# Optimization experiments

Measured on AMD Instinct MI355X. Metric: run time of the kernel, lower is better.

Reference implementation:

```python
import jax, jax.numpy as jnp
import numpy as np

NUM_CLASSES = 90
NUM_ANCHORS = 9          # 3 octaves x 3 aspect ratios
MAX_DETECTION_POINTS = 5000
MAX_DET_PER_IMAGE = 100
SIGMA = 0.5              # gaussian soft-NMS sigma
IMAGE_SIZE = 512
LEVEL_HW = [64, 32, 16, 8, 4]   # levels 3..7, stride 8..128
BATCH = 16


def _make_anchors():
    """effdet-style anchors, [N,4] in (y1,x1,y2,x2) pixel coords, per-location
    anchor-contiguous ordering (matches permute(0,2,3,1) flattening)."""
    boxes_all = []
    for level in range(3, 8):
        stride = 2 ** level
        boxes_level = []
        for octave in range(3):
            for aspect in (1.0, 2.0, 0.5):
                base = 4.0 * stride * 2.0 ** (octave / 3.0)  # anchor_scale=4
                ax = np.sqrt(aspect)
                ay = 1.0 / ax
                hx = base * ax / 2.0
                hy = base * ay / 2.0
                xs = np.arange(stride / 2.0, IMAGE_SIZE, stride)
                xv, yv = np.meshgrid(xs, xs)
                b = np.stack([yv - hy, xv - hx, yv + hy, xv + hx], axis=-1)
                boxes_level.append(b.reshape(-1, 1, 4))
        boxes_all.append(np.concatenate(boxes_level, axis=1).reshape(-1, 4))
    return np.concatenate(boxes_all, axis=0).astype(np.float32)


def setup_inputs() -> dict:
    key = jax.random.key(0)
    ks = jax.random.split(key, 10)
    inp = {}
    for i, hw in enumerate(LEVEL_HW):
        inp[f"cls_l{i}"] = jax.random.normal(ks[i], (BATCH, NUM_ANCHORS * NUM_CLASSES, hw, hw), jnp.float32)
        inp[f"box_l{i}"] = jax.random.normal(ks[5 + i], (BATCH, NUM_ANCHORS * 4, hw, hw), jnp.float32) * 0.1
    inp["anchors"] = jnp.asarray(_make_anchors())
    return inp


def _flatten_level(t, c):
    # [B, A*c, H, W] -> [B, H*W*A, c]
    B, _, H, W = t.shape
    return jnp.transpose(t, (0, 2, 3, 1)).reshape(B, H * W * NUM_ANCHORS, c)


def _iou(box, boxes):
    # box [4], boxes [N,4], xyxy
    x1 = jnp.maximum(box[0], boxes[:, 0])
    y1 = jnp.maximum(box[1], boxes[:, 1])
    x2 = jnp.minimum(box[2], boxes[:, 2])
    y2 = jnp.minimum(box[3], boxes[:, 3])
    inter = jnp.clip(x2 - x1, 0.0) * jnp.clip(y2 - y1, 0.0)
    a1 = (box[2] - box[0]) * (box[3] - box[1])
    a2 = (boxes[:, 2] - boxes[:, 0]) * (boxes[:, 3] - boxes[:, 1])
    return inter / (a1 + a2 - inter + 1e-8)


def _soft_nms(bx, sc, cl):
    # gaussian soft-NMS: iteratively pick max score, decay neighbours.
    def step(sc_work, _):
        i = jnp.argmax(sc_work)
        s = sc_work[i]
        ious = _iou(bx[i], bx)
        decay = jnp.exp(-(ious * ious) / SIGMA)
        sc_new = (sc_work * decay).at[i].set(-jnp.inf)
        return sc_new, (i, s)

    _, (idxs, sels) = jax.lax.scan(step, sc, None, length=MAX_DET_PER_IMAGE)
    # detections [max_det, 6] = x1,y1,x2,y2,score,class
    return jnp.concatenate(
        [bx[idxs], sels[:, None], cl[idxs].astype(jnp.float32)[:, None]], axis=1)


def reference(cls_l0, cls_l1, cls_l2, cls_l3, cls_l4,
              box_l0, box_l1, box_l2, box_l3, box_l4, anchors):
    cls_levels = [cls_l0, cls_l1, cls_l2, cls_l3, cls_l4]
    box_levels = [box_l0, box_l1, box_l2, box_l3, box_l4]
    B = cls_l0.shape[0]

    cls_all = jnp.concatenate([_flatten_level(t, NUM_CLASSES) for t in cls_levels], 1)  # [B,N,C]
    box_all = jnp.concatenate([_flatten_level(t, 4) for t in box_levels], 1)            # [B,N,4]

    # top-k over flattened anchor*class logits (effdet _post_process)
    top_scores, top_idx = jax.lax.top_k(cls_all.reshape(B, -1), MAX_DETECTION_POINTS)
    anchor_idx = top_idx // NUM_CLASSES    # [B,K]
    classes = top_idx % NUM_CLASSES        # [B,K]

    rel = jnp.take_along_axis(box_all, anchor_idx[..., None], axis=1)  # [B,K,4]
    anc = anchors[anchor_idx]                                          # [B,K,4] (y1,x1,y2,x2)
    scores = jax.nn.sigmoid(top_scores)

    # decode (effdet decode_box_outputs, output xyxy)
    ya = (anc[..., 0] + anc[..., 2]) * 0.5
    xa = (anc[..., 1] + anc[..., 3]) * 0.5
    ha = anc[..., 2] - anc[..., 0]
    wa = anc[..., 3] - anc[..., 1]
    ty, tx, th, tw = rel[..., 0], rel[..., 1], rel[..., 2], rel[..., 3]
    w = jnp.exp(tw) * wa
    h = jnp.exp(th) * ha
    yc = ty * ha + ya
    xc = tx * wa + xa
    boxes = jnp.stack([xc - w * 0.5, yc - h * 0.5, xc + w * 0.5, yc + h * 0.5], -1)

    return jax.vmap(_soft_nms)(boxes, scores, classes)  # [B, max_det, 6]
```

## Files before the change

### kernel.cpp

```cpp
#include <hip/hip_runtime.h>
#include <math.h>

#define K_TOP   5000
#define M_HOT   2048
#define NHOT    2560
#define NSEL2   5632
#define MAX_DET 100
#define CAP     16384
#define SCAP    384
#define NSH     64
#define TAU     2.8f
#define BATCH   16

__device__ __forceinline__ unsigned f2u(float x) {
    unsigned b = __float_as_uint(x);
    return (b & 0x80000000u) ? ~b : (b | 0x80000000u);
}
__device__ __forceinline__ float u2f(unsigned u) {
    unsigned b = (u & 0x80000000u) ? (u & 0x7fffffffu) : ~u;
    return __uint_as_float(b);
}

__global__ __launch_bounds__(256) void k_compact(
    const float* __restrict__ c0, const float* __restrict__ c1,
    const float* __restrict__ c2, const float* __restrict__ c3,
    const float* __restrict__ c4,
    unsigned* __restrict__ ctr, uint2* __restrict__ cbuf)
{
    const unsigned V0 = 13271040u, V1 = 16588800u, V2 = 17418240u,
                   V3 = 17625600u, V4 = 17677440u;
    unsigned tid  = threadIdx.x;
    unsigned lane = tid & 63u;
    unsigned wid  = tid >> 6;
    unsigned shard = (blockIdx.x * 4u + wid) & (NSH - 1u);
    unsigned gbase = blockIdx.x * 2048u + tid;

    #pragma unroll 1
    for (int it = 0; it < 8; it++) {
        unsigned g = gbase + (unsigned)it * 256u;
        bool valid = (g < V4);
        const float* p; unsigned vbase, lgHW, lgW, aoff;
        if (g < V0)      { p = c0; vbase = 0;  lgHW = 12; lgW = 6; aoff = 0; }
        else if (g < V1) { p = c1; vbase = V0; lgHW = 10; lgW = 5; aoff = 36864u; }
        else if (g < V2) { p = c2; vbase = V1; lgHW = 8;  lgW = 4; aoff = 46080u; }
        else if (g < V3) { p = c3; vbase = V2; lgHW = 6;  lgW = 3; aoff = 48384u; }
        else             { p = c4; vbase = V3; lgHW = 4;  lgW = 2; aoff = 48960u; }

        unsigned us[4], fl[4];
        int m = 0;
        unsigned b = 0;
        if (valid) {
            unsigned elem = (g - vbase) << 2;
            unsigned pos  = elem & ((1u << lgHW) - 1u);
            unsigned q    = elem >> lgHW;
            b             = q / 810u;
            unsigned ch   = q - b * 810u;
            unsigned a    = ch / 90u;
            unsigned c    = ch - a * 90u;
            unsigned h    = pos >> lgW;
            unsigned w0   = pos & ((1u << lgW) - 1u);
            float4 v = *(const float4*)(p + elem);
            unsigned anch = aoff + ((h << lgW) + w0) * 9u + a;
            float vv[4] = {v.x, v.y, v.z, v.w};
            #pragma unroll
            for (int k = 0; k < 4; k++) {
                if (vv[k] > TAU) {
                    us[m] = f2u(vv[k]);
                    fl[m] = (anch + (unsigned)k * 9u) * 90u + c;
                    m++;
                }
            }
        }

        unsigned bb  = valid ? b : 0xffffffffu;
        unsigned b0u = (unsigned)__shfl((int)bb, 0);
        unsigned long long same = __ballot(bb == b0u);
        if (same == ~0ULL) {
            unsigned long long B[4];
            int cnt[4];
            #pragma unroll
            for (int k = 0; k < 4; k++) { B[k] = __ballot(m > k); cnt[k] = __popcll(B[k]); }
            int tot = cnt[0] + cnt[1] + cnt[2] + cnt[3];
            if (tot > 0) {
                unsigned base = 0;
                if (lane == 0)
                    base = atomicAdd(&ctr[(b0u * NSH + shard) * 16u], (unsigned)tot);
                base = (unsigned)__shfl((int)base, 0);
                unsigned long long below = (lane == 0) ? 0ULL : ((1ULL << lane) - 1ULL);
                unsigned lb = 0;
                #pragma unroll
                for (int k = 0; k < 4; k++) {
                    if (k < m) {
                        unsigned o = base + lb + (unsigned)__popcll(B[k] & below);
                        if (o < SCAP)
                            cbuf[((size_t)b0u * NSH + shard) * SCAP + o] = make_uint2(us[k], fl[k]);
                    }
                    lb += (unsigned)cnt[k];
                }
            }
        } else {
            for (int k = 0; k < m; k++) {
                unsigned o = atomicAdd(&ctr[(b * NSH + shard) * 16u], 1u);
                if (o < SCAP)
                    cbuf[((size_t)b * NSH + shard) * SCAP + o] = make_uint2(us[k], fl[k]);
            }
        }
    }
}

__global__ __launch_bounds__(1024) void k_select(
    const uint2* __restrict__ cbuf, const unsigned* __restrict__ ctr,
    uint2* __restrict__ tmp,
    const float* __restrict__ b0p, const float* __restrict__ b1p,
    const float* __restrict__ b2p, const float* __restrict__ b3p,
    const float* __restrict__ b4p, const float* __restrict__ anchors,
    float* __restrict__ sx1, float* __restrict__ sy1,
    float* __restrict__ sx2, float* __restrict__ sy2,
    float* __restrict__ ssc, float* __restrict__ scl,
    unsigned* __restrict__ su, unsigned* __restrict__ sfl,
    float* __restrict__ u2sig_arr)
{
    int img = blockIdx.x;
    int tid = threadIdx.x;
    unsigned lane = (unsigned)tid & 63u;
    __shared__ unsigned hist[256];
    __shared__ unsigned scnt[NSH], spref[NSH];
    __shared__ unsigned sTot;
    __shared__ unsigned sPrefix, sNeed;
    __shared__ unsigned cE, cH, cC;

    for (int i = tid; i < NSEL2; i += 1024) {
        size_t o = (size_t)img * NSEL2 + i;
        ssc[o] = -INFINITY;
        sx1[o] = 0.f; sy1[o] = 0.f; sx2[o] = 0.f; sy2[o] = 0.f; scl[o] = 0.f;
        su[o] = 0u; sfl[o] = 0xffffffffu;
    }

    if (tid < NSH) {
        unsigned c = ctr[((unsigned)img * NSH + (unsigned)tid) * 16u];
        scnt[tid] = (c > SCAP) ? SCAP : c;
    }
    __syncthreads();
    if (tid == 0) {
        unsigned s = 0;
        for (int i = 0; i < NSH; i++) { spref[i] = s; s += scnt[i]; }
        sTot = (s > CAP) ? CAP : s;
    }
    __syncthreads();
    for (unsigned idx = (unsigned)tid; idx < NSH * SCAP; idx += 1024u) {
        unsigned sh = idx / SCAP, j = idx - sh * SCAP;
        if (j < scnt[sh]) {
            unsigned dst = spref[sh] + j;
            if (dst < CAP)
                tmp[(size_t)img * CAP + dst] = cbuf[((size_t)img * NSH + sh) * SCAP + j];
        }
    }
    __syncthreads();
    unsigned n = sTot;
    const uint2* buf = tmp + (size_t)img * CAP;

    unsigned uthr[2], needArr[2];
    #pragma unroll 1
    for (int si = 0; si < 2; si++) {
        unsigned prefix = 0, need = (si == 0) ? K_TOP : M_HOT;
        for (int r = 0; r < 4; r++) {
            int sh = 24 - 8 * r;
            for (int i = tid; i < 256; i += 1024) hist[i] = 0;
            __syncthreads();
            for (unsigned i0 = 0; i0 < n; i0 += 1024) {
                unsigned i = i0 + (unsigned)tid;
                bool vld = false; unsigned bin = 0;
                if (i < n) {
                    unsigned u = buf[i].x;
                    vld = (r == 0) || ((u >> (sh + 8)) == prefix);
                    bin = (u >> sh) & 0xffu;
                }
                unsigned long long act = __ballot(vld);
                if (act) {
                    int fa = __ffsll(act) - 1;
                    unsigned fb = (unsigned)__shfl((int)bin, fa);
                    unsigned long long sm = __ballot(vld && (bin == fb));
                    if (sm == act) {
                        if ((int)lane == fa) atomicAdd(&hist[fb], (unsigned)__popcll(act));
                    } else if (vld) {
                        atomicAdd(&hist[bin], 1u);
                    }
                }
            }
            __syncthreads();
            if (tid == 0) {
                unsigned s = 0; int bin = 255;
                for (; bin > 0; bin--) {
                    unsigned t = s + hist[bin];
                    if (t >= need) break;
                    s = t;
                }
                sPrefix = (prefix << 8) | (unsigned)bin;
                sNeed   = need - s;
            }
            __syncthreads();
            prefix = sPrefix;
            need   = sNeed;
        }
        uthr[si] = prefix; needArr[si] = need;
    }
    unsigned u_star = uthr[0], needEq = needArr[0];
    unsigned u2key  = uthr[1];
    if (n <= K_TOP) { u_star = 0; needEq = K_TOP; }
    if (n <= M_HOT) { u2key = 0; }

    if (tid == 0) {
        cE = 0; cH = 0; cC = 0;
        u2sig_arr[img] = (n > M_HOT) ? 1.0f / (1.0f + expf(-u2f(u2key))) : -1.0f;
    }
    __syncthreads();

    for (unsigned i0 = 0; i0 < n; i0 += 1024) {
        unsigned i = i0 + (unsigned)tid;
        unsigned u = 0, fx = 0;
        bool gt = false, eq = false;
        if (i < n) {
            uint2 e = buf[i];
            u = e.x; fx = e.y;
            gt = (u > u_star);
            eq = (u == u_star);
        }
        bool win = gt;
        unsigned long long me = __ballot(eq);
        if (me) {
            int leader = __ffsll(me) - 1;
            unsigned base = 0;
            if ((int)lane == leader) base = atomicAdd(&cE, (unsigned)__popcll(me));
            base = (unsigned)__shfl((int)base, leader);
            if (eq) {
                unsigned qd = base + (unsigned)__popcll(me & ((1ULL << lane) - 1ULL));
                if (qd < needEq) win = true;
            }
        }
        bool hot = win && (u >= u2key);
        unsigned dest = 0xffffffffu;
        bool spill = false;
        unsigned long long mh = __ballot(hot);
        if (mh) {
            int leader = __ffsll(mh) - 1;
            unsigned base = 0;
            if ((int)lane == leader) base = atomicAdd(&cH, (unsigned)__popcll(mh));
            base = (unsigned)__shfl((int)base, leader);
            if (hot) {
                unsigned hq = base + (unsigned)__popcll(mh & ((1ULL << lane) - 1ULL));
                if (hq < NHOT) dest = hq; else spill = true;
            }
        }
        bool cold = win && (!hot || spill);
        unsigned long long mc = __ballot(cold);
        if (mc) {
            int leader = __ffsll(mc) - 1;
            unsigned base = 0;
            if ((int)lane == leader) base = atomicAdd(&cC, (unsigned)__popcll(mc));
            base = (unsigned)__shfl((int)base, leader);
            if (cold) dest = NHOT + base + (unsigned)__popcll(mc & ((1ULL << lane) - 1ULL));
        }
        if (win && dest < NSEL2) {
            unsigned anchor = fx / 90u;
            unsigned c      = fx - anchor * 90u;
            const float* bp; unsigned off, lgW;
            if (anchor < 36864u)      { bp = b0p; off = 0;      lgW = 6; }
            else if (anchor < 46080u) { bp = b1p; off = 36864u; lgW = 5; }
            else if (anchor < 48384u) { bp = b2p; off = 46080u; lgW = 4; }
            else if (anchor < 48960u) { bp = b3p; off = 48384u; lgW = 3; }
            else                      { bp = b4p; off = 48960u; lgW = 2; }
            unsigned il   = anchor - off;
            unsigned a    = il % 9u;
            unsigned ppos = il / 9u;
            unsigned w    = ppos & ((1u << lgW) - 1u);
            unsigned h    = ppos >> lgW;
            unsigned HW   = 1u << (2 * lgW);
            size_t base_i = ((size_t)((unsigned)img * 36u + a * 4u) << (2 * lgW))
                            + ((size_t)h << lgW) + w;
            float ty  = bp[base_i];
            float tx  = bp[base_i + HW];
            float th  = bp[base_i + 2 * (size_t)HW];
            float tw_ = bp[base_i + 3 * (size_t)HW];
            float4 anc = ((const float4*)anchors)[anchor];
            float ya = (anc.x + anc.z) * 0.5f;
            float xa = (anc.y + anc.w) * 0.5f;
            float ha = anc.z - anc.x;
            float wa = anc.w - anc.y;
            float wb = expf(tw_) * wa;
            float hb = expf(th)  * ha;
            float yc = ty * ha + ya;
            float xc = tx * wa + xa;
            float logit = u2f(u);
            float score = 1.0f / (1.0f + expf(-logit));
            size_t o = (size_t)img * NSEL2 + dest;
            sx1[o] = xc - wb * 0.5f;
            sy1[o] = yc - hb * 0.5f;
            sx2[o] = xc + wb * 0.5f;
            sy2[o] = yc + hb * 0.5f;
            ssc[o] = score;
            scl[o] = (float)c;
            su[o]  = u;
            sfl[o] = fx;
        }
    }
}

template<int NS>
__device__ __forceinline__ float nms_run(
    const float* __restrict__ sx1, const float* __restrict__ sy1,
    const float* __restrict__ sx2, const float* __restrict__ sy2,
    const float* __restrict__ ssc, const float* __restrict__ scl,
    const unsigned* __restrict__ su, const unsigned* __restrict__ sfl,
    float* __restrict__ out, int img,
    float* shv, int* shs, unsigned long long* shk, float* bbx)
{
    int tid = threadIdx.x;
    unsigned lane = (unsigned)tid & 63u;
    unsigned wid  = (unsigned)tid >> 6;

    float x1[NS], y1[NS], x2[NS], y2[NS], sc[NS], cl[NS], ar[NS];
    unsigned long long kk[NS];
    size_t base = (size_t)img * NSEL2;
    #pragma unroll
    for (int j = 0; j < NS; j++) {
        int s = tid + j * 256;
        x1[j] = sx1[base + s]; y1[j] = sy1[base + s];
        x2[j] = sx2[base + s]; y2[j] = sy2[base + s];
        sc[j] = ssc[base + s]; cl[j] = scl[base + s];
        kk[j] = ((unsigned long long)su[base + s] << 32)
              | (unsigned long long)(0xffffffffu - sfl[base + s]);
        ar[j] = (x2[j] - x1[j]) * (y2[j] - y1[j]);
    }

    float last = -INFINITY;
    for (int it = 0; it < MAX_DET; it++) {
        float v = sc[0]; int s = tid; unsigned long long k = kk[0];
        #pragma unroll
        for (int j = 1; j < NS; j++) {
            if (sc[j] > v || (sc[j] == v && kk[j] > k)) {
                v = sc[j]; s = tid + j * 256; k = kk[j];
            }
        }
        #pragma unroll
        for (int d = 32; d; d >>= 1) {
            float v2 = __shfl_down(v, d);
            int   s2 = __shfl_down(s, d);
            unsigned long long k2 = __shfl_down(k, d);
            if (v2 > v || (v2 == v && k2 > k)) { v = v2; s = s2; k = k2; }
        }
        if (lane == 0) { shv[wid] = v; shs[wid] = s; shk[wid] = k; }
        __syncthreads();
        v = shv[0]; s = shs[0]; k = shk[0];
        #pragma unroll
        for (int w = 1; w < 4; w++) {
            float v2 = shv[w]; int s2 = shs[w]; unsigned long long k2 = shk[w];
            if (v2 > v || (v2 == v && k2 > k)) { v = v2; s = s2; k = k2; }
        }
        int ot = s & 255, oj = s >> 8;
        if (tid == ot) {
            float* bx = bbx;
            #pragma unroll
            for (int j = 0; j < NS; j++) {
                if (j == oj) {
                    bx[0] = x1[j]; bx[1] = y1[j]; bx[2] = x2[j]; bx[3] = y2[j];
                    bx[4] = cl[j];
                    sc[j] = -INFINITY;
                }
            }
        }
        __syncthreads();
        float gx1 = bbx[0], gy1 = bbx[1], gx2 = bbx[2], gy2 = bbx[3];
        if (tid == 0) {
            float* o = out + ((size_t)img * MAX_DET + it) * 6;
            o[0] = gx1; o[1] = gy1; o[2] = gx2; o[3] = gy2;
            o[4] = v;  o[5] = bbx[4];
        }
        last = v;
        float ga = (gx2 - gx1) * (gy2 - gy1);
        #pragma unroll
        for (int j = 0; j < NS; j++) {
            float xx1 = fmaxf(gx1, x1[j]);
            float yy1 = fmaxf(gy1, y1[j]);
            float xx2 = fminf(gx2, x2[j]);
            float yy2 = fminf(gy2, y2[j]);
            float inter = fmaxf(xx2 - xx1, 0.f) * fmaxf(yy2 - yy1, 0.f);
            float iou = inter / (ga + ar[j] - inter + 1e-8f);
            sc[j] *= expf(-2.0f * iou * iou);
        }
    }
    return last;
}

__global__ __launch_bounds__(256) void k_nms(
    const float* __restrict__ sx1, const float* __restrict__ sy1,
    const float* __restrict__ sx2, const float* __restrict__ sy2,
    const float* __restrict__ ssc, const float* __restrict__ scl,
    const unsigned* __restrict__ su, const unsigned* __restrict__ sfl,
    const float* __restrict__ u2sig_arr,
    float* __restrict__ out)
{
    __shared__ float shv[4];
    __shared__ int shs[4];
    __shared__ unsigned long long shk[4];
    __shared__ float bbx[5];
    int img = blockIdx.x;

    float s100 = nms_run<10>(sx1, sy1, sx2, sy2, ssc, scl, su, sfl,
                             out, img, shv, shs, shk, bbx);
    float u2s = u2sig_arr[img];
    if (!(s100 > u2s)) {
        __syncthreads();
        nms_run<22>(sx1, sy1, sx2, sy2, ssc, scl, su, sfl,
                    out, img, shv, shs, shk, bbx);
    }
}

extern "C" void kernel_launch(void* const* d_in, const int* in_sizes, int n_in,
                              void* d_out, int out_size, void* d_ws, size_t ws_size,
                              hipStream_t stream)
{
    const float* cls[5] = {0,0,0,0,0};
    const float* box[5] = {0,0,0,0,0};
    const float* anchors = 0;
    const int cls_sz[5] = {53084160, 13271040, 3317760, 829440, 207360};
    const int box_sz[5] = {2359296, 589824, 147456, 36864, 9216};
    for (int i = 0; i < n_in; i++) {
        int sz = in_sizes[i];
        const float* p = (const float*)d_in[i];
        if (sz == 196416) { anchors = p; continue; }
        for (int l = 0; l < 5; l++) {
            if (sz == cls_sz[l]) { cls[l] = p; break; }
            if (sz == box_sz[l]) { box[l] = p; break; }
        }
    }
    float* out = (float*)d_out;

    char* ws = (char*)d_ws;
    unsigned* ctr = (unsigned*)ws;
    size_t off = (size_t)BATCH * NSH * 16 * sizeof(unsigned);
    float* u2sig = (float*)(ws + off);
    off += 256;
    uint2* cbuf = (uint2*)(ws + off);
    off += (size_t)BATCH * NSH * SCAP * sizeof(uint2);
    uint2* tmp = (uint2*)(ws + off);
    off += (size_t)BATCH * CAP * sizeof(uint2);
    float* sel = (float*)(ws + off);
    float* sx1 = sel;
    float* sy1 = sel + 1 * (size_t)BATCH * NSEL2;
    float* sx2 = sel + 2 * (size_t)BATCH * NSEL2;
    float* sy2 = sel + 3 * (size_t)BATCH * NSEL2;
    float* ssc = sel + 4 * (size_t)BATCH * NSEL2;
    float* scl = sel + 5 * (size_t)BATCH * NSEL2;
    unsigned* su  = (unsigned*)(sel + 6 * (size_t)BATCH * NSEL2);
    unsigned* sfl = (unsigned*)(sel + 7 * (size_t)BATCH * NSEL2);

    hipMemsetAsync(ctr, 0, (size_t)BATCH * NSH * 16 * sizeof(unsigned), stream);
    k_compact<<<dim3(8632), dim3(256), 0, stream>>>(cls[0], cls[1], cls[2], cls[3], cls[4],
                                                    ctr, cbuf);
    k_select<<<dim3(BATCH), dim3(1024), 0, stream>>>(cbuf, ctr, tmp,
                                                     box[0], box[1], box[2], box[3], box[4],
                                                     anchors,
                                                     sx1, sy1, sx2, sy2, ssc, scl, su, sfl,
                                                     u2sig);
    k_nms<<<dim3(BATCH), dim3(256), 0, stream>>>(sx1, sy1, sx2, sy2, ssc, scl, su, sfl,
                                                 u2sig, out);
}
```

Measured before the change: 730.7 us.

## Run hot-set soft-NMS in a single wavefront with DPP argmax reduction

The fast-path soft-NMS now runs in one 64-lane wavefront per image, holding a smaller hot candidate set (M_HOT 2048 to 1024) in registers. The argmax uses DPP cross-lane ops and readlane broadcasts, which removes the LDS round-trips and __syncthreads per iteration. The fallback full-set NMS moves to a separate kernel gated by a per-image flag, at the cost of an extra launch and higher register pressure (17 slots of 9 arrays per lane). A smaller hot set may also trigger the fallback more often, and the fallback is costly.

```diff
diff --git a/kernel.cpp b/kernel.cpp
--- a/kernel.cpp
+++ b/kernel.cpp
@@ -2,9 +2,11 @@
 #include <math.h>
 
 #define K_TOP   5000
-#define M_HOT   2048
-#define NHOT    2560
-#define NSEL2   5632
+#define M_HOT   1024
+#define NHOT    1088
+#define NSEL2   5696
+#define NS_HOT  17
+#define NS_FIX  23
 #define MAX_DET 100
 #define CAP     16384
 #define SCAP    384
@@ -305,80 +307,87 @@
     }
 }
 
-template<int NS>
-__device__ __forceinline__ float nms_run(
+template<int CTRL, int RM>
+__device__ __forceinline__ void dpp_amax(float& v, int& s, unsigned& kh, unsigned& kl) {
+    float v2 = __int_as_float(__builtin_amdgcn_update_dpp(
+        __float_as_int(v), __float_as_int(v), CTRL, RM, 0xf, false));
+    int s2 = __builtin_amdgcn_update_dpp(s, s, CTRL, RM, 0xf, false);
+    unsigned h2 = (unsigned)__builtin_amdgcn_update_dpp((int)kh, (int)kh, CTRL, RM, 0xf, false);
+    unsigned l2 = (unsigned)__builtin_amdgcn_update_dpp((int)kl, (int)kl, CTRL, RM, 0xf, false);
+    bool better = (v2 > v) || (v2 == v && (h2 > kh || (h2 == kh && l2 > kl)));
+    if (better) { v = v2; s = s2; kh = h2; kl = l2; }
+}
+
+__global__ __launch_bounds__(64) void k_nms(
     const float* __restrict__ sx1, const float* __restrict__ sy1,
     const float* __restrict__ sx2, const float* __restrict__ sy2,
     const float* __restrict__ ssc, const float* __restrict__ scl,
     const unsigned* __restrict__ su, const unsigned* __restrict__ sfl,
-    float* __restrict__ out, int img,
-    float* shv, int* shs, unsigned long long* shk, float* bbx)
+    const float* __restrict__ u2sig_arr, unsigned* __restrict__ flags,
+    float* __restrict__ out)
 {
+    int img = blockIdx.x;
     int tid = threadIdx.x;
-    unsigned lane = (unsigned)tid & 63u;
-    unsigned wid  = (unsigned)tid >> 6;
-
-    float x1[NS], y1[NS], x2[NS], y2[NS], sc[NS], cl[NS], ar[NS];
-    unsigned long long kk[NS];
+
+    float x1[NS_HOT], y1[NS_HOT], x2[NS_HOT], y2[NS_HOT], sc[NS_HOT], cl[NS_HOT], ar[NS_HOT];
+    unsigned kh[NS_HOT], kl[NS_HOT];
     size_t base = (size_t)img * NSEL2;
     #pragma unroll
-    for (int j = 0; j < NS; j++) {
-        int s = tid + j * 256;
+    for (int j = 0; j < NS_HOT; j++) {
+        int s = tid + j * 64;
         x1[j] = sx1[base + s]; y1[j] = sy1[base + s];
         x2[j] = sx2[base + s]; y2[j] = sy2[base + s];
         sc[j] = ssc[base + s]; cl[j] = scl[base + s];
-        kk[j] = ((unsigned long long)su[base + s] << 32)
-              | (unsigned long long)(0xffffffffu - sfl[base + s]);
+        kh[j] = su[base + s];  kl[j] = ~sfl[base + s];
         ar[j] = (x2[j] - x1[j]) * (y2[j] - y1[j]);
     }
 
     float last = -INFINITY;
+    #pragma unroll 1
     for (int it = 0; it < MAX_DET; it++) {
-        float v = sc[0]; int s = tid; unsigned long long k = kk[0];
-        #pragma unroll
-        for (int j = 1; j < NS; j++) {
-            if (sc[j] > v || (sc[j] == v && kk[j] > k)) {
-                v = sc[j]; s = tid + j * 256; k = kk[j];
-            }
-        }
-        #pragma unroll
-        for (int d = 32; d; d >>= 1) {
-            float v2 = __shfl_down(v, d);
-            int   s2 = __shfl_down(s, d);
-            unsigned long long k2 = __shfl_down(k, d);
-            if (v2 > v || (v2 == v && k2 > k)) { v = v2; s = s2; k = k2; }
-        }
-        if (lane == 0) { shv[wid] = v; shs[wid] = s; shk[wid] = k; }
-        __syncthreads();
-        v = shv[0]; s = shs[0]; k = shk[0];
-        #pragma unroll
-        for (int w = 1; w < 4; w++) {
-            float v2 = shv[w]; int s2 = shs[w]; unsigned long long k2 = shk[w];
-            if (v2 > v || (v2 == v && k2 > k)) { v = v2; s = s2; k = k2; }
-        }
-        int ot = s & 255, oj = s >> 8;
-        if (tid == ot) {
-            float* bx = bbx;
-            #pragma unroll
-            for (int j = 0; j < NS; j++) {
-                if (j == oj) {
-                    bx[0] = x1[j]; bx[1] = y1[j]; bx[2] = x2[j]; bx[3] = y2[j];
-                    bx[4] = cl[j];
-                    sc[j] = -INFINITY;
-                }
-            }
-        }
-        __syncthreads();
-        float gx1 = bbx[0], gy1 = bbx[1], gx2 = bbx[2], gy2 = bbx[3];
-        if (tid == 0) {
+        float v = sc[0]; int s = tid; unsigned bh = kh[0], bl = kl[0];
+        #pragma unroll
+        for (int j = 1; j < NS_HOT; j++) {
+            bool better = (sc[j] > v) ||
+                          (sc[j] == v && (kh[j] > bh || (kh[j] == bh && kl[j] > bl)));
+            if (better) { v = sc[j]; s = tid + j * 64; bh = kh[j]; bl = kl[j]; }
+        }
+        dpp_amax<0x111, 0xf>(v, s, bh, bl);
+        dpp_amax<0x112, 0xf>(v, s, bh, bl);
+        dpp_amax<0x114, 0xf>(v, s, bh, bl);
+        dpp_amax<0x118, 0xf>(v, s, bh, bl);
+        dpp_amax<0x142, 0xa>(v, s, bh, bl);
+        dpp_amax<0x143, 0xc>(v, s, bh, bl);
+
+        int wslot = __builtin_amdgcn_readlane(s, 63);
+        float wv  = __int_as_float(__builtin_amdgcn_readlane(__float_as_int(v), 63));
+        wslot = __builtin_amdgcn_readfirstlane(wslot);
+        int wj    = wslot >> 6;
+        int owner = wslot & 63;
+
+        float rx1 = 0.f, ry1 = 0.f, rx2 = 0.f, ry2 = 0.f, rcl = 0.f;
+        #pragma unroll
+        for (int j = 0; j < NS_HOT; j++) {
+            if (j == wj) {
+                rx1 = x1[j]; ry1 = y1[j]; rx2 = x2[j]; ry2 = y2[j]; rcl = cl[j];
+                if (tid == owner) sc[j] = -INFINITY;
+            }
+        }
+        float gx1 = __int_as_float(__builtin_amdgcn_readlane(__float_as_int(rx1), owner));
+        float gy1 = __int_as_float(__builtin_amdgcn_readlane(__float_as_int(ry1), owner));
+        float gx2 = __int_as_float(__builtin_amdgcn_readlane(__float_as_int(rx2), owner));
+        float gy2 = __int_as_float(__builtin_amdgcn_readlane(__float_as_int(ry2), owner));
+
+        if (tid == owner) {
             float* o = out + ((size_t)img * MAX_DET + it) * 6;
-            o[0] = gx1; o[1] = gy1; o[2] = gx2; o[3] = gy2;
-            o[4] = v;  o[5] = bbx[4];
-        }
-        last = v;
+            o[0] = rx1; o[1] = ry1; o[2] = rx2; o[3] = ry2;
+            o[4] = wv;  o[5] = rcl;
+        }
+        last = wv;
+
         float ga = (gx2 - gx1) * (gy2 - gy1);
         #pragma unroll
-        for (int j = 0; j < NS; j++) {
+        for (int j = 0; j < NS_HOT; j++) {
             float xx1 = fmaxf(gx1, x1[j]);
             float yy1 = fmaxf(gy1, y1[j]);
             float xx2 = fminf(gx2, x2[j]);
@@ -388,30 +397,105 @@
             sc[j] *= expf(-2.0f * iou * iou);
         }
     }
-    return last;
-}
-
-__global__ __launch_bounds__(256) void k_nms(
+
+    if (tid == 0) {
+        float u2s = u2sig_arr[img];
+        flags[img] = (last > u2s) ? 0u : 1u;
+    }
+}
+
+__global__ __launch_bounds__(256) void k_fix(
     const float* __restrict__ sx1, const float* __restrict__ sy1,
     const float* __restrict__ sx2, const float* __restrict__ sy2,
     const float* __restrict__ ssc, const float* __restrict__ scl,
     const unsigned* __restrict__ su, const unsigned* __restrict__ sfl,
-    const float* __restrict__ u2sig_arr,
+    const unsigned* __restrict__ flags,
     float* __restrict__ out)
 {
+    int img = blockIdx.x;
+    if (flags[img] == 0) return;
+    int tid = threadIdx.x;
+    unsigned lane = (unsigned)tid & 63u;
+    unsigned wid  = (unsigned)tid >> 6;
+
     __shared__ float shv[4];
-    __shared__ int shs[4];
+    __shared__ int   shs[4];
     __shared__ unsigned long long shk[4];
     __shared__ float bbx[5];
-    int img = blockIdx.x;
-
-    float s100 = nms_run<10>(sx1, sy1, sx2, sy2, ssc, scl, su, sfl,
-                             out, img, shv, shs, shk, bbx);
-    float u2s = u2sig_arr[img];
-    if (!(s100 > u2s)) {
+
+    float x1[NS_FIX], y1[NS_FIX], x2[NS_FIX], y2[NS_FIX], sc[NS_FIX], cl[NS_FIX], ar[NS_FIX];
+    unsigned long long kk[NS_FIX];
+    size_t base = (size_t)img * NSEL2;
+    #pragma unroll
+    for (int j = 0; j < NS_FIX; j++) {
+        int s = tid + j * 256;
+        if (s < NSEL2) {
+            x1[j] = sx1[base + s]; y1[j] = sy1[base + s];
+            x2[j] = sx2[base + s]; y2[j] = sy2[base + s];
+            sc[j] = ssc[base + s]; cl[j] = scl[base + s];
+            kk[j] = ((unsigned long long)su[base + s] << 32)
+                  | (unsigned long long)(~sfl[base + s]);
+        } else {
+            x1[j] = 0.f; y1[j] = 0.f; x2[j] = 0.f; y2[j] = 0.f;
+            sc[j] = -INFINITY; cl[j] = 0.f; kk[j] = 0ULL;
+        }
+        ar[j] = (x2[j] - x1[j]) * (y2[j] - y1[j]);
+    }
+
+    #pragma unroll 1
+    for (int it = 0; it < MAX_DET; it++) {
+        float v = sc[0]; int s = tid; unsigned long long k = kk[0];
+        #pragma unroll
+        for (int j = 1; j < NS_FIX; j++) {
+            if (sc[j] > v || (sc[j] == v && kk[j] > k)) {
+                v = sc[j]; s = tid + j * 256; k = kk[j];
+            }
+        }
+        #pragma unroll
+        for (int d = 32; d; d >>= 1) {
+            float v2 = __shfl_down(v, d);
+            int   s2 = __shfl_down(s, d);
+            unsigned long long k2 = __shfl_down(k, d);
+            if (v2 > v || (v2 == v && k2 > k)) { v = v2; s = s2; k = k2; }
+        }
+        if (lane == 0) { shv[wid] = v; shs[wid] = s; shk[wid] = k; }
         __syncthreads();
-        nms_run<22>(sx1, sy1, sx2, sy2, ssc, scl, su, sfl,
-                    out, img, shv, shs, shk, bbx);
+        v = shv[0]; s = shs[0]; k = shk[0];
+        #pragma unroll
+        for (int w = 1; w < 4; w++) {
+            float v2 = shv[w]; int s2 = shs[w]; unsigned long long k2 = shk[w];
+            if (v2 > v || (v2 == v && k2 > k)) { v = v2; s = s2; k = k2; }
+        }
+        int ot = s & 255, oj = s >> 8;
+        if (tid == ot) {
+            #pragma unroll
+            for (int j = 0; j < NS_FIX; j++) {
+                if (j == oj) {
+                    bbx[0] = x1[j]; bbx[1] = y1[j]; bbx[2] = x2[j]; bbx[3] = y2[j];
+                    bbx[4] = cl[j];
+                    sc[j] = -INFINITY;
+                }
+            }
+        }
+        __syncthreads();
+        float gx1 = bbx[0], gy1 = bbx[1], gx2 = bbx[2], gy2 = bbx[3];
+        if (tid == 0) {
+            float* o = out + ((size_t)img * MAX_DET + it) * 6;
+            o[0] = gx1; o[1] = gy1; o[2] = gx2; o[3] = gy2;
+            o[4] = v;   o[5] = bbx[4];
+        }
+        float ga = (gx2 - gx1) * (gy2 - gy1);
+        #pragma unroll
+        for (int j = 0; j < NS_FIX; j++) {
+            float xx1 = fmaxf(gx1, x1[j]);
+            float yy1 = fmaxf(gy1, y1[j]);
+            float xx2 = fminf(gx2, x2[j]);
+            float yy2 = fminf(gy2, y2[j]);
+            float inter = fmaxf(xx2 - xx1, 0.f) * fmaxf(yy2 - yy1, 0.f);
+            float iou = inter / (ga + ar[j] - inter + 1e-8f);
+            sc[j] *= expf(-2.0f * iou * iou);
+        }
+        __syncthreads();
     }
 }
 
@@ -438,7 +522,8 @@
     char* ws = (char*)d_ws;
     unsigned* ctr = (unsigned*)ws;
     size_t off = (size_t)BATCH * NSH * 16 * sizeof(unsigned);
-    float* u2sig = (float*)(ws + off);
+    float*    u2sig = (float*)(ws + off);
+    unsigned* flags = (unsigned*)(ws + off + 64);
     off += 256;
     uint2* cbuf = (uint2*)(ws + off);
     off += (size_t)BATCH * NSH * SCAP * sizeof(uint2);
@@ -462,6 +547,8 @@
                                                      anchors,
                                                      sx1, sy1, sx2, sy2, ssc, scl, su, sfl,
                                                      u2sig);
-    k_nms<<<dim3(BATCH), dim3(256), 0, stream>>>(sx1, sy1, sx2, sy2, ssc, scl, su, sfl,
-                                                 u2sig, out);
-}
+    k_nms<<<dim3(BATCH), dim3(64), 0, stream>>>(sx1, sy1, sx2, sy2, ssc, scl, su, sfl,
+                                                u2sig, flags, out);
+    k_fix<<<dim3(BATCH), dim3(256), 0, stream>>>(sx1, sy1, sx2, sy2, ssc, scl, su, sfl,
+                                                 flags, out);
+}
```

Result: slower. 1.201 ms (+64.4%).
